# Performance work log

Measured on AMD Instinct MI355X. Metric: run time of the kernel, lower is better.

Reference implementation:

```python
import jax, jax.numpy as jnp
import numpy as np
import math

N = 50000      # nodes
E = 800000     # edges
D = 128        # in/out channels (hidden_dim)
H = 16         # heads
C = D // H     # per-head channels = 8
DH = 4 * D     # mlp hidden = 512
EPS = 1e-5


def layernorm(x, g, b):
    mu = jnp.mean(x, axis=-1, keepdims=True)
    var = jnp.var(x, axis=-1, keepdims=True)
    return (x - mu) * jax.lax.rsqrt(var + EPS) * g + b


def setup_inputs() -> dict:
    key = jax.random.key(0)
    ks = jax.random.split(key, 16)
    s = lambda k, shape, fan: jax.random.normal(k, shape, jnp.float32) / np.sqrt(fan)
    inp = {
        "x": jax.random.normal(ks[0], (N, D), jnp.float32),
        "edge_index": jax.random.randint(ks[1], (2, E), 0, N, jnp.int32),
        "edge_attr": jax.random.normal(ks[2], (E, D), jnp.float32),
        # layer norm 1
        "ln1_g": jnp.ones((D,), jnp.float32), "ln1_b": jnp.zeros((D,), jnp.float32),
        # q/k/v/self projections (in=D, out=H*C=D)
        "wq": s(ks[3], (D, D), D), "bq": jnp.zeros((D,), jnp.float32),
        "wk": s(ks[4], (D, D), D), "bk": jnp.zeros((D,), jnp.float32),
        "wv": s(ks[5], (D, D), D), "bv": jnp.zeros((D,), jnp.float32),
        "ws": s(ks[6], (D, D), D), "bs": jnp.zeros((D,), jnp.float32),
        # edge projection (edge_dim=D -> H*C)
        "we": s(ks[7], (D, D), D), "be": jnp.zeros((D,), jnp.float32),
        # output projection
        "wp": s(ks[8], (D, D), D), "bp": jnp.zeros((D,), jnp.float32),
        # node_dst_mlp: LN -> Linear(D,4D) -> SiLU -> Linear(4D,D)
        "mlp_ln_g": jnp.ones((D,), jnp.float32), "mlp_ln_b": jnp.zeros((D,), jnp.float32),
        "w1": s(ks[9], (D, DH), D), "b1": jnp.zeros((DH,), jnp.float32),
        "w2": s(ks[10], (DH, D), DH), "b2": jnp.zeros((D,), jnp.float32),
    }
    return inp


def reference(x, edge_index, edge_attr, ln1_g, ln1_b, wq, bq, wk, bk, wv, bv,
              ws, bs, we, be, wp, bp, mlp_ln_g, mlp_ln_b, w1, b1, w2, b2):
    src, dst = edge_index[0], edge_index[1]  # message j -> i

    h = layernorm(x, ln1_g, ln1_b)
    q = (h @ wq + bq).reshape(N, H, C)
    k = (h @ wk + bk).reshape(N, H, C)
    v = (h @ wv + bv).reshape(N, H, C)
    x_r = h @ ws + bs                         # [N, D]

    # per-edge gather + edge-feature add
    k_j = k[src] + (edge_attr @ we + be).reshape(E, H, C)  # [E,H,C]
    alpha = jnp.sum(q[dst] * k_j, axis=-1) / math.sqrt(C)  # [E,H]

    # segment softmax over destination nodes
    m = jax.ops.segment_max(alpha, dst, num_segments=N)    # [N,H]
    ex = jnp.exp(alpha - m[dst])
    denom = jax.ops.segment_sum(ex, dst, num_segments=N)   # [N,H]
    alpha = ex / denom[dst]

    # weighted scatter-add aggregation
    msg = v[src] * alpha[..., None]                        # [E,H,C]
    agg = jax.ops.segment_sum(msg, dst, num_segments=N).reshape(N, D)

    out = (agg + x_r) @ wp + bp
    out = out + x                                          # residual to raw input
    mlp_out = jax.nn.silu(layernorm(out, mlp_ln_g, mlp_ln_b) @ w1 + b1) @ w2 + b2
    return mlp_out + out
```

## Files before the change

kernel.cpp:

```cpp
#include <hip/hip_runtime.h>

#define N_NODES 50000
#define N_EDGES 800000
#define D 128
#define H 16
#define DH 512

typedef __attribute__((ext_vector_type(8))) short short8;
typedef __attribute__((ext_vector_type(4))) float f32x4;

static __device__ __forceinline__ unsigned short f2bf(float f) {
    unsigned u = __float_as_uint(f);
    u += 0x7FFF + ((u >> 16) & 1);
    return (unsigned short)(u >> 16);
}
static __device__ __forceinline__ float bf2f(unsigned short u) {
    return __uint_as_float(((unsigned)u) << 16);
}

__global__ void ln_kernel(const float* __restrict__ x, const float* __restrict__ g,
                          const float* __restrict__ b, unsigned short* __restrict__ out, int n) {
    int w = (blockIdx.x * blockDim.x + threadIdx.x) >> 6;
    int lane = threadIdx.x & 63;
    if (w >= n) return;
    float2 v = *(const float2*)(x + (size_t)w * D + lane * 2);
    float s = v.x + v.y, ss = v.x * v.x + v.y * v.y;
#pragma unroll
    for (int off = 32; off; off >>= 1) { s += __shfl_xor(s, off); ss += __shfl_xor(ss, off); }
    float mean = s * (1.0f / D);
    float var = ss * (1.0f / D) - mean * mean;
    float rstd = rsqrtf(var + 1e-5f);
    float2 gv = *(const float2*)(g + lane * 2);
    float2 bv = *(const float2*)(b + lane * 2);
    ushort2 o;
    o.x = f2bf((v.x - mean) * rstd * gv.x + bv.x);
    o.y = f2bf((v.y - mean) * rstd * gv.y + bv.y);
    *(ushort2*)(out + (size_t)w * D + lane * 2) = o;
}

__global__ void prep_kernel(const float* __restrict__ wq, const float* __restrict__ wk,
                            const float* __restrict__ wv, const float* __restrict__ ws,
                            const float* __restrict__ we, const float* __restrict__ wp,
                            const float* __restrict__ w1, const float* __restrict__ w2,
                            const float* __restrict__ bq, const float* __restrict__ bk,
                            const float* __restrict__ bv, const float* __restrict__ bs,
                            unsigned short* __restrict__ wqkvsT, unsigned short* __restrict__ weT,
                            unsigned short* __restrict__ wpT, unsigned short* __restrict__ w1T,
                            unsigned short* __restrict__ w2T, float* __restrict__ bias_qkvs) {
    int idx = blockIdx.x * blockDim.x + threadIdx.x;
    if (idx < 65536) {
        int seg = idx >> 14, r = idx & 16383;
        const float* src = seg == 0 ? wq : seg == 1 ? wk : seg == 2 ? wv : ws;
        int o = r >> 7, i = r & 127;
        wqkvsT[idx] = f2bf(src[i * 128 + o]);
    } else if (idx < 81920) {
        int r = idx - 65536; int o = r >> 7, i = r & 127;
        weT[r] = f2bf(we[i * 128 + o]);
    } else if (idx < 98304) {
        int r = idx - 81920; int o = r >> 7, i = r & 127;
        wpT[r] = f2bf(wp[i * 128 + o]);
    } else if (idx < 163840) {
        int r = idx - 98304; int o = r >> 7, i = r & 127;
        w1T[r] = f2bf(w1[i * 512 + o]);
    } else if (idx < 229376) {
        int r = idx - 163840; int o = r >> 9, i = r & 511;
        w2T[r] = f2bf(w2[i * 128 + o]);
    } else if (idx < 229888) {
        int r = idx - 229376;
        const float* p = r < 128 ? bq : r < 256 ? bk : r < 384 ? bv : bs;
        bias_qkvs[r] = p[r & 127];
    }
}

__global__ void hist_kernel(const int* __restrict__ edge_index, int* __restrict__ counts) {
    int e = blockIdx.x * blockDim.x + threadIdx.x;
    if (e < N_EDGES) atomicAdd(&counts[edge_index[N_EDGES + e]], 1);
}

__global__ void scan1_kernel(const int* __restrict__ counts, int* __restrict__ excl,
                             int* __restrict__ bsum) {
    __shared__ int sm[1024];
    int b = blockIdx.x, tid = threadIdx.x;
    int idx = b * 1024 + tid;
    int v = (idx < N_NODES) ? counts[idx] : 0;
    sm[tid] = v;
    __syncthreads();
    for (int off = 1; off < 1024; off <<= 1) {
        int t = (tid >= off) ? sm[tid - off] : 0;
        __syncthreads();
        sm[tid] += t;
        __syncthreads();
    }
    if (idx < N_NODES) excl[idx] = sm[tid] - v;
    if (tid == 1023) bsum[b] = sm[1023];
}

__global__ void scan2_kernel(int* __restrict__ bsum, int nb) {
    if (threadIdx.x == 0 && blockIdx.x == 0) {
        int run = 0;
        for (int i = 0; i < nb; ++i) { int v = bsum[i]; bsum[i] = run; run += v; }
    }
}

__global__ void scan3_kernel(const int* __restrict__ excl, const int* __restrict__ bsum,
                             int* __restrict__ row_ptr, int* __restrict__ cursor) {
    int b = blockIdx.x, tid = threadIdx.x;
    int idx = b * 1024 + tid;
    if (idx < N_NODES) {
        int v = bsum[b] + excl[idx];
        row_ptr[idx] = v;
        cursor[idx] = v;
    }
    if (idx == 0) row_ptr[N_NODES] = N_EDGES;
}

__global__ void scatter_kernel(const int* __restrict__ edge_index, int* __restrict__ cursor,
                               int* __restrict__ slot_of, int* __restrict__ src_ord) {
    int e = blockIdx.x * blockDim.x + threadIdx.x;
    if (e < N_EDGES) {
        int dst = edge_index[N_EDGES + e];
        int pos = atomicAdd(&cursor[dst], 1);
        slot_of[e] = pos;
        src_ord[pos] = edge_index[e];
    }
}

enum { EPI_F32 = 0, EPI_RESID = 1, EPI_SILU_BF = 2, EPI_ADDOUT = 3, EPI_BF16 = 4 };

template <int KD, int EPI>
__global__ void gemm_kernel(const unsigned short* __restrict__ A, const unsigned short* __restrict__ BT,
                            const float* __restrict__ bias, void* __restrict__ outp,
                            const float* __restrict__ extra, int M, int Nout) {
    int wave = threadIdx.x >> 6, lane = threadIdx.x & 63;
    int lr = lane & 15, lq = lane >> 4;
    int row0 = (blockIdx.x * 4 + wave) * 16;
    int col0 = blockIdx.y * 64;
    int arow = row0 + lr;
    if (arow >= M) arow = M - 1;
    f32x4 z = {0.f, 0.f, 0.f, 0.f};
    f32x4 acc[4] = {z, z, z, z};
#pragma unroll
    for (int t = 0; t < KD / 32; ++t) {
        short8 a = *(const short8*)(A + (size_t)arow * KD + t * 32 + lq * 8);
#pragma unroll
        for (int cf = 0; cf < 4; ++cf) {
            short8 b = *(const short8*)(BT + (size_t)(col0 + cf * 16 + lr) * KD + t * 32 + lq * 8);
            acc[cf] = __builtin_amdgcn_mfma_f32_16x16x32_bf16(a, b, acc[cf], 0, 0, 0);
        }
    }
#pragma unroll
    for (int cf = 0; cf < 4; ++cf) {
        int col = col0 + cf * 16 + lr;
        float bv = bias[col];
#pragma unroll
        for (int r = 0; r < 4; ++r) {
            int row = row0 + lq * 4 + r;
            if (row >= M) continue;
            float v = acc[cf][r] + bv;
            if (EPI == EPI_F32) {
                ((float*)outp)[(size_t)row * Nout + col] = v;
            } else if (EPI == EPI_RESID) {
                ((float*)outp)[(size_t)row * Nout + col] = v + extra[(size_t)row * D + col];
            } else if (EPI == EPI_SILU_BF) {
                float sg = 1.0f / (1.0f + __expf(-v));
                ((unsigned short*)outp)[(size_t)row * Nout + col] = f2bf(v * sg);
            } else if (EPI == EPI_ADDOUT) {
                ((float*)outp)[(size_t)row * Nout + col] = v + extra[(size_t)row * D + col];
            } else {
                ((unsigned short*)outp)[(size_t)row * Nout + col] = f2bf(v);
            }
        }
    }
}

__global__ __launch_bounds__(128)
void edge_score_kernel(const float* __restrict__ edge_attr,
                       const unsigned short* __restrict__ weT,
                       const float* __restrict__ be, const int* __restrict__ edge_index,
                       const int* __restrict__ slot_of,
                       const unsigned short* __restrict__ qkvs,
                       float* __restrict__ qE) {
    __shared__ unsigned short q_lds[32][132];
    __shared__ float s_lds[32][20];
    int wave = threadIdx.x >> 6, lane = threadIdx.x & 63;
    int lr = lane & 15, lq = lane >> 4;
    int w16 = wave * 16;
    int e0w = blockIdx.x * 32 + w16;

    int dstv = edge_index[N_EDGES + e0w + lr];
    int slotv = slot_of[e0w + lr];

    int plane = lane >> 5, h2 = lane & 31;
#pragma unroll
    for (int it = 0; it < 8; ++it) {
        int row16 = it * 2 + plane;
        int dst = __shfl(dstv, row16);
        *(ushort4*)(&q_lds[w16 + row16][h2 * 4]) =
            *(const ushort4*)(qkvs + (size_t)dst * 512 + h2 * 4);
    }

    short8 a[4];
#pragma unroll
    for (int t = 0; t < 4; ++t) {
        const f32x4* p = (const f32x4*)(edge_attr + (size_t)(e0w + lr) * D + t * 32 + lq * 8);
        f32x4 lo = __builtin_nontemporal_load(p);
        f32x4 hi = __builtin_nontemporal_load(p + 1);
        short8 av;
        av[0] = f2bf(lo[0]); av[1] = f2bf(lo[1]); av[2] = f2bf(lo[2]); av[3] = f2bf(lo[3]);
        av[4] = f2bf(hi[0]); av[5] = f2bf(hi[1]); av[6] = f2bf(hi[2]); av[7] = f2bf(hi[3]);
        a[t] = av;
    }
    f32x4 z = {0.f, 0.f, 0.f, 0.f};
    f32x4 acc[8] = {z, z, z, z, z, z, z, z};
#pragma unroll
    for (int cf = 0; cf < 8; ++cf) {
#pragma unroll
        for (int t = 0; t < 4; ++t) {
            short8 b = *(const short8*)(weT + (size_t)(cf * 16 + lr) * D + t * 32 + lq * 8);
            acc[cf] = __builtin_amdgcn_mfma_f32_16x16x32_bf16(a[t], b, acc[cf], 0, 0, 0);
        }
    }

#pragma unroll
    for (int cf = 0; cf < 8; ++cf) {
        int col = cf * 16 + lr;
        float bev = be[col];
#pragma unroll
        for (int r = 0; r < 4; ++r) {
            int el = w16 + lq * 4 + r;
            float qv = bf2f(q_lds[el][col]);
            float p = qv * (acc[cf][r] + bev);
            p += __shfl_xor(p, 1);
            p += __shfl_xor(p, 2);
            p += __shfl_xor(p, 4);
            if ((lr & 7) == 0)
                s_lds[el][cf * 2 + (lr >> 3)] = p;
        }
    }

    int el16 = lane >> 2;
    int slot = __shfl(slotv, el16);
    f32x4 sv = *(const f32x4*)(&s_lds[w16 + el16][(lane & 3) * 4]);
    *(f32x4*)(qE + (size_t)slot * 16 + (lane & 3) * 4) = sv;
}

__global__ void agg_kernel(const int* __restrict__ row_ptr, const int* __restrict__ src_ord,
                           const float* __restrict__ qE, const unsigned short* __restrict__ qkvs,
                           unsigned short* __restrict__ aggxr) {
    int w = (blockIdx.x * blockDim.x + threadIdx.x) >> 6;
    int lane = threadIdx.x & 63;
    if (w >= N_NODES) return;
    int c = lane * 2, h = lane >> 2;
    int s = row_ptr[w], e = row_ptr[w + 1], deg = e - s;
    int src_p = (lane < deg) ? src_ord[s + lane] : 0;
    ushort2 q2 = *(const ushort2*)(qkvs + (size_t)w * 512 + c);
    float qa = bf2f(q2.x), qb = bf2f(q2.y);
    const float scale = 0.35355339059327373f;
    float acc0 = 0.f, acc1 = 0.f, den = 0.f;
    for (int i = 0; i < deg; ++i) {
        int src = (i < 64) ? __shfl(src_p, i) : src_ord[s + i];
        ushort2 k2 = *(const ushort2*)(qkvs + (size_t)src * 512 + 128 + c);
        ushort2 v2 = *(const ushort2*)(qkvs + (size_t)src * 512 + 256 + c);
        float pa = qa * bf2f(k2.x) + qb * bf2f(k2.y);
        pa += __shfl_xor(pa, 1);
        pa += __shfl_xor(pa, 2);
        float qEv = qE[(size_t)(s + i) * 16 + h];
        float ex = __expf((pa + qEv) * scale);
        acc0 += ex * bf2f(v2.x);
        acc1 += ex * bf2f(v2.y);
        den += ex;
    }
    float inv = den > 0.f ? 1.0f / den : 0.f;
    ushort2 x2 = *(const ushort2*)(qkvs + (size_t)w * 512 + 384 + c);
    ushort2 o;
    o.x = f2bf(acc0 * inv + bf2f(x2.x));
    o.y = f2bf(acc1 * inv + bf2f(x2.y));
    *(ushort2*)(aggxr + (size_t)w * D + c) = o;
}

extern "C" void kernel_launch(void* const* d_in, const int* in_sizes, int n_in,
                              void* d_out, int out_size, void* d_ws, size_t ws_size,
                              hipStream_t stream) {
    const float* x = (const float*)d_in[0];
    const int* edge_index = (const int*)d_in[1];
    const float* edge_attr = (const float*)d_in[2];
    const float* ln1_g = (const float*)d_in[3];
    const float* ln1_b = (const float*)d_in[4];
    const float* wq = (const float*)d_in[5];  const float* bq = (const float*)d_in[6];
    const float* wk = (const float*)d_in[7];  const float* bk = (const float*)d_in[8];
    const float* wv = (const float*)d_in[9];  const float* bv = (const float*)d_in[10];
    const float* wsw = (const float*)d_in[11]; const float* bs = (const float*)d_in[12];
    const float* we = (const float*)d_in[13]; const float* be = (const float*)d_in[14];
    const float* wp = (const float*)d_in[15]; const float* bp = (const float*)d_in[16];
    const float* mlp_g = (const float*)d_in[17]; const float* mlp_b = (const float*)d_in[18];
    const float* w1 = (const float*)d_in[19]; const float* b1 = (const float*)d_in[20];
    const float* w2 = (const float*)d_in[21]; const float* b2 = (const float*)d_in[22];

    char* base = (char*)d_ws;
    size_t off = 0;
    auto alloc = [&](size_t bytes) -> char* {
        char* p = base + off;
        off = (off + bytes + 255) & ~(size_t)255;
        return p;
    };
    unsigned short* qkvs   = (unsigned short*)alloc((size_t)N_NODES * 512 * 2);
    float* qE_buf          = (float*)alloc((size_t)N_EDGES * H * 4);
    unsigned short* h_bf   = (unsigned short*)alloc((size_t)N_NODES * D * 2);
    unsigned short* aggxr  = (unsigned short*)alloc((size_t)N_NODES * D * 2);
    float* outbuf          = (float*)alloc((size_t)N_NODES * D * 4);
    unsigned short* ln2_bf = (unsigned short*)alloc((size_t)N_NODES * D * 2);
    unsigned short* silu_bf= (unsigned short*)alloc((size_t)N_NODES * DH * 2);
    int* counts            = (int*)alloc((size_t)N_NODES * 4);
    int* row_ptr           = (int*)alloc((size_t)(N_NODES + 1) * 4);
    int* cursor            = (int*)alloc((size_t)N_NODES * 4);
    int* slot_of           = (int*)alloc((size_t)N_EDGES * 4);
    int* src_ord           = (int*)alloc((size_t)N_EDGES * 4);
    int* excl              = (int*)alloc((size_t)N_NODES * 4);
    int* bsum              = (int*)alloc(64 * 4);
    unsigned short* wqkvsT = (unsigned short*)alloc(512 * 128 * 2);
    unsigned short* weT    = (unsigned short*)alloc(128 * 128 * 2);
    unsigned short* wpT    = (unsigned short*)alloc(128 * 128 * 2);
    unsigned short* w1T    = (unsigned short*)alloc(512 * 128 * 2);
    unsigned short* w2T    = (unsigned short*)alloc(128 * 512 * 2);
    float* bias_qkvs       = (float*)alloc(512 * 4);

    const int NB = (N_NODES + 1023) / 1024;

    prep_kernel<<<898, 256, 0, stream>>>(wq, wk, wv, wsw, we, wp, w1, w2, bq, bk, bv, bs,
                                         wqkvsT, weT, wpT, w1T, w2T, bias_qkvs);

    (void)hipMemsetAsync(counts, 0, (size_t)N_NODES * 4, stream);
    hist_kernel<<<(N_EDGES + 255) / 256, 256, 0, stream>>>(edge_index, counts);
    scan1_kernel<<<NB, 1024, 0, stream>>>(counts, excl, bsum);
    scan2_kernel<<<1, 64, 0, stream>>>(bsum, NB);
    scan3_kernel<<<NB, 1024, 0, stream>>>(excl, bsum, row_ptr, cursor);
    scatter_kernel<<<(N_EDGES + 255) / 256, 256, 0, stream>>>(edge_index, cursor, slot_of, src_ord);

    ln_kernel<<<(N_NODES + 3) / 4, 256, 0, stream>>>(x, ln1_g, ln1_b, h_bf, N_NODES);

    dim3 g_node((N_NODES + 63) / 64, 8);
    gemm_kernel<128, EPI_BF16><<<g_node, 256, 0, stream>>>(h_bf, wqkvsT, bias_qkvs, qkvs, nullptr, N_NODES, 512);

    edge_score_kernel<<<N_EDGES / 32, 128, 0, stream>>>(edge_attr, weT, be, edge_index, slot_of, qkvs, qE_buf);

    agg_kernel<<<(N_NODES + 3) / 4, 256, 0, stream>>>(row_ptr, src_ord, qE_buf, qkvs, aggxr);

    dim3 g_out((N_NODES + 63) / 64, 2);
    gemm_kernel<128, EPI_RESID><<<g_out, 256, 0, stream>>>(aggxr, wpT, bp, outbuf, x, N_NODES, 128);

    ln_kernel<<<(N_NODES + 3) / 4, 256, 0, stream>>>(outbuf, mlp_g, mlp_b, ln2_bf, N_NODES);

    dim3 g_mlp1((N_NODES + 63) / 64, 8);
    gemm_kernel<128, EPI_SILU_BF><<<g_mlp1, 256, 0, stream>>>(ln2_bf, w1T, b1, silu_bf, nullptr, N_NODES, 512);

    dim3 g_mlp2((N_NODES + 63) / 64, 2);
    gemm_kernel<512, EPI_ADDOUT><<<g_mlp2, 256, 0, stream>>>(silu_bf, w2T, b2, (float*)d_out, outbuf, N_NODES, 128);
}
```

Before: 676.3 us.

## Split edge projection GEMM from score computation into two kernels

The fused edge-score kernel is split in two. One kernel runs the edge_attr @ we GEMM, processing 32 rows per wave, and writes a bf16 intermediate E_bf. A second kernel gathers q[dst], adds the bias, computes per-head dot products and scatters the scores to their CSR slots. The intent is to simplify each kernel and improve MFMA/occupancy, at the cost of writing and re-reading a 200MB bf16 intermediate. Rounding E to bf16 before the bias add and dot product also slightly changes numerics.

After: 737.7 us. 1.09x slower.

```diff
diff --git a/kernel.cpp b/kernel.cpp
--- a/kernel.cpp
+++ b/kernel.cpp
@@ -173,75 +173,78 @@
     }
 }
 
-__global__ __launch_bounds__(128)
-void edge_score_kernel(const float* __restrict__ edge_attr,
-                       const unsigned short* __restrict__ weT,
-                       const float* __restrict__ be, const int* __restrict__ edge_index,
-                       const int* __restrict__ slot_of,
-                       const unsigned short* __restrict__ qkvs,
-                       float* __restrict__ qE) {
-    __shared__ unsigned short q_lds[32][132];
-    __shared__ float s_lds[32][20];
+__global__ __launch_bounds__(256)
+void e_gemm_kernel(const float* __restrict__ edge_attr,
+                   const unsigned short* __restrict__ weT,
+                   unsigned short* __restrict__ E_bf) {
     int wave = threadIdx.x >> 6, lane = threadIdx.x & 63;
     int lr = lane & 15, lq = lane >> 4;
-    int w16 = wave * 16;
-    int e0w = blockIdx.x * 32 + w16;
-
-    int dstv = edge_index[N_EDGES + e0w + lr];
-    int slotv = slot_of[e0w + lr];
-
-    int plane = lane >> 5, h2 = lane & 31;
-#pragma unroll
-    for (int it = 0; it < 8; ++it) {
-        int row16 = it * 2 + plane;
-        int dst = __shfl(dstv, row16);
-        *(ushort4*)(&q_lds[w16 + row16][h2 * 4]) =
-            *(const ushort4*)(qkvs + (size_t)dst * 512 + h2 * 4);
-    }
-
-    short8 a[4];
+    int row0 = (blockIdx.x * 4 + wave) * 32;
+
+    short8 a0[4], a1[4];
 #pragma unroll
     for (int t = 0; t < 4; ++t) {
-        const f32x4* p = (const f32x4*)(edge_attr + (size_t)(e0w + lr) * D + t * 32 + lq * 8);
-        f32x4 lo = __builtin_nontemporal_load(p);
-        f32x4 hi = __builtin_nontemporal_load(p + 1);
-        short8 av;
-        av[0] = f2bf(lo[0]); av[1] = f2bf(lo[1]); av[2] = f2bf(lo[2]); av[3] = f2bf(lo[3]);
-        av[4] = f2bf(hi[0]); av[5] = f2bf(hi[1]); av[6] = f2bf(hi[2]); av[7] = f2bf(hi[3]);
-        a[t] = av;
+        const f32x4* p0 = (const f32x4*)(edge_attr + (size_t)(row0 + lr) * D + t * 32 + lq * 8);
+        const f32x4* p1 = (const f32x4*)(edge_attr + (size_t)(row0 + 16 + lr) * D + t * 32 + lq * 8);
+        f32x4 lo0 = __builtin_nontemporal_load(p0);
+        f32x4 hi0 = __builtin_nontemporal_load(p0 + 1);
+        f32x4 lo1 = __builtin_nontemporal_load(p1);
+        f32x4 hi1 = __builtin_nontemporal_load(p1 + 1);
+        short8 v0, v1;
+        v0[0] = f2bf(lo0[0]); v0[1] = f2bf(lo0[1]); v0[2] = f2bf(lo0[2]); v0[3] = f2bf(lo0[3]);
+        v0[4] = f2bf(hi0[0]); v0[5] = f2bf(hi0[1]); v0[6] = f2bf(hi0[2]); v0[7] = f2bf(hi0[3]);
+        v1[0] = f2bf(lo1[0]); v1[1] = f2bf(lo1[1]); v1[2] = f2bf(lo1[2]); v1[3] = f2bf(lo1[3]);
+        v1[4] = f2bf(hi1[0]); v1[5] = f2bf(hi1[1]); v1[6] = f2bf(hi1[2]); v1[7] = f2bf(hi1[3]);
+        a0[t] = v0; a1[t] = v1;
     }
     f32x4 z = {0.f, 0.f, 0.f, 0.f};
-    f32x4 acc[8] = {z, z, z, z, z, z, z, z};
+    f32x4 acc0[8] = {z, z, z, z, z, z, z, z};
+    f32x4 acc1[8] = {z, z, z, z, z, z, z, z};
 #pragma unroll
     for (int cf = 0; cf < 8; ++cf) {
 #pragma unroll
         for (int t = 0; t < 4; ++t) {
             short8 b = *(const short8*)(weT + (size_t)(cf * 16 + lr) * D + t * 32 + lq * 8);
-            acc[cf] = __builtin_amdgcn_mfma_f32_16x16x32_bf16(a[t], b, acc[cf], 0, 0, 0);
+            acc0[cf] = __builtin_amdgcn_mfma_f32_16x16x32_bf16(a0[t], b, acc0[cf], 0, 0, 0);
+            acc1[cf] = __builtin_amdgcn_mfma_f32_16x16x32_bf16(a1[t], b, acc1[cf], 0, 0, 0);
         }
     }
-
 #pragma unroll
     for (int cf = 0; cf < 8; ++cf) {
         int col = cf * 16 + lr;
-        float bev = be[col];
 #pragma unroll
         for (int r = 0; r < 4; ++r) {
-            int el = w16 + lq * 4 + r;
-            float qv = bf2f(q_lds[el][col]);
-            float p = qv * (acc[cf][r] + bev);
-            p += __shfl_xor(p, 1);
-            p += __shfl_xor(p, 2);
-            p += __shfl_xor(p, 4);
-            if ((lr & 7) == 0)
-                s_lds[el][cf * 2 + (lr >> 3)] = p;
+            int row = row0 + lq * 4 + r;
+            E_bf[(size_t)row * D + col] = f2bf(acc0[cf][r]);
+            E_bf[(size_t)(row + 16) * D + col] = f2bf(acc1[cf][r]);
         }
     }
-
-    int el16 = lane >> 2;
-    int slot = __shfl(slotv, el16);
-    f32x4 sv = *(const f32x4*)(&s_lds[w16 + el16][(lane & 3) * 4]);
-    *(f32x4*)(qE + (size_t)slot * 16 + (lane & 3) * 4) = sv;
+}
+
+__global__ __launch_bounds__(256)
+void score_kernel(const unsigned short* __restrict__ E_bf, const float* __restrict__ be,
+                  const int* __restrict__ edge_index, const int* __restrict__ slot_of,
+                  const unsigned short* __restrict__ qkvs, float* __restrict__ qE) {
+    int gw = (blockIdx.x * blockDim.x + threadIdx.x) >> 6;
+    int lane = threadIdx.x & 63;
+    int c2 = lane * 2, h = lane >> 2;
+    int base_e = gw * 16;
+    int dstv = edge_index[N_EDGES + base_e + (lane & 15)];
+    int slotv = slot_of[base_e + (lane & 15)];
+    float2 bev = *(const float2*)(be + c2);
+#pragma unroll
+    for (int i = 0; i < 16; ++i) {
+        int e = base_e + i;
+        int dst = __shfl(dstv, i);
+        int slot = __shfl(slotv, i);
+        ushort2 q2 = *(const ushort2*)(qkvs + (size_t)dst * 512 + c2);
+        ushort2 E2 = *(const ushort2*)(E_bf + (size_t)e * D + c2);
+        float p = bf2f(q2.x) * (bf2f(E2.x) + bev.x) + bf2f(q2.y) * (bf2f(E2.y) + bev.y);
+        p += __shfl_xor(p, 1);
+        p += __shfl_xor(p, 2);
+        if ((lane & 3) == 0)
+            qE[(size_t)slot * 16 + h] = p;
+    }
 }
 
 __global__ void agg_kernel(const int* __restrict__ row_ptr, const int* __restrict__ src_ord,
@@ -305,6 +308,7 @@
     };
     unsigned short* qkvs   = (unsigned short*)alloc((size_t)N_NODES * 512 * 2);
     float* qE_buf          = (float*)alloc((size_t)N_EDGES * H * 4);
+    unsigned short* E_bf   = (unsigned short*)alloc((size_t)N_EDGES * D * 2);
     unsigned short* h_bf   = (unsigned short*)alloc((size_t)N_NODES * D * 2);
     unsigned short* aggxr  = (unsigned short*)alloc((size_t)N_NODES * D * 2);
     float* outbuf          = (float*)alloc((size_t)N_NODES * D * 4);
@@ -341,7 +345,8 @@
     dim3 g_node((N_NODES + 63) / 64, 8);
     gemm_kernel<128, EPI_BF16><<<g_node, 256, 0, stream>>>(h_bf, wqkvsT, bias_qkvs, qkvs, nullptr, N_NODES, 512);
 
-    edge_score_kernel<<<N_EDGES / 32, 128, 0, stream>>>(edge_attr, weT, be, edge_index, slot_of, qkvs, qE_buf);
+    e_gemm_kernel<<<N_EDGES / 128, 256, 0, stream>>>(edge_attr, weT, E_bf);
+    score_kernel<<<N_EDGES / 64, 256, 0, stream>>>(E_bf, be, edge_index, slot_of, qkvs, qE_buf);
 
     agg_kernel<<<(N_NODES + 3) / 4, 256, 0, stream>>>(row_ptr, src_ord, qE_buf, qkvs, aggxr);
 
```

## Fuse layernorms into GEMMs, interleave K/V layout, prefetch edge loads

Applied to the files above, without the earlier changes.

Removes both standalone layernorm kernels and computes LN inside the GEMM A-tile load, so the normalized bf16 intermediates are never written to or read back from memory. Each of the 8 column blocks recomputes the LN of the same fp32 rows, which adds redundant reads and math. The QKVS output is stored with K and V interleaved per channel, so the aggregation loop fetches both with one ushort4 load instead of two. In the edge score kernel, the edge_attr loads and q gathers are issued into registers before the LDS stores, to overlap their memory latency.

Result: slower. 711.7 us (+5.2%).

```diff
diff --git a/kernel.cpp b/kernel.cpp
--- a/kernel.cpp
+++ b/kernel.cpp
@@ -16,26 +16,6 @@
 }
 static __device__ __forceinline__ float bf2f(unsigned short u) {
     return __uint_as_float(((unsigned)u) << 16);
-}
-
-__global__ void ln_kernel(const float* __restrict__ x, const float* __restrict__ g,
-                          const float* __restrict__ b, unsigned short* __restrict__ out, int n) {
-    int w = (blockIdx.x * blockDim.x + threadIdx.x) >> 6;
-    int lane = threadIdx.x & 63;
-    if (w >= n) return;
-    float2 v = *(const float2*)(x + (size_t)w * D + lane * 2);
-    float s = v.x + v.y, ss = v.x * v.x + v.y * v.y;
-#pragma unroll
-    for (int off = 32; off; off >>= 1) { s += __shfl_xor(s, off); ss += __shfl_xor(ss, off); }
-    float mean = s * (1.0f / D);
-    float var = ss * (1.0f / D) - mean * mean;
-    float rstd = rsqrtf(var + 1e-5f);
-    float2 gv = *(const float2*)(g + lane * 2);
-    float2 bv = *(const float2*)(b + lane * 2);
-    ushort2 o;
-    o.x = f2bf((v.x - mean) * rstd * gv.x + bv.x);
-    o.y = f2bf((v.y - mean) * rstd * gv.y + bv.y);
-    *(ushort2*)(out + (size_t)w * D + lane * 2) = o;
 }
 
 __global__ void prep_kernel(const float* __restrict__ wq, const float* __restrict__ wk,
@@ -125,7 +105,7 @@
     }
 }
 
-enum { EPI_F32 = 0, EPI_RESID = 1, EPI_SILU_BF = 2, EPI_ADDOUT = 3, EPI_BF16 = 4 };
+enum { EPI_F32 = 0, EPI_RESID = 1, EPI_SILU_BF = 2, EPI_ADDOUT = 3, EPI_BF16 = 4, EPI_QKVS = 5 };
 
 template <int KD, int EPI>
 __global__ void gemm_kernel(const unsigned short* __restrict__ A, const unsigned short* __restrict__ BT,
@@ -173,6 +153,83 @@
     }
 }
 
+template <int EPI>
+__global__ void gemm_ln_kernel(const float* __restrict__ A, const unsigned short* __restrict__ BT,
+                               const float* __restrict__ bias, const float* __restrict__ lng,
+                               const float* __restrict__ lnb, void* __restrict__ outp,
+                               int M, int Nout) {
+    int wave = threadIdx.x >> 6, lane = threadIdx.x & 63;
+    int lr = lane & 15, lq = lane >> 4;
+    int row0 = (blockIdx.x * 4 + wave) * 16;
+    int col0 = blockIdx.y * 64;
+    int arow = row0 + lr;
+    if (arow >= M) arow = M - 1;
+
+    f32x4 xa[8];
+    float s = 0.f, ss = 0.f;
+#pragma unroll
+    for (int t = 0; t < 4; ++t) {
+        const f32x4* p = (const f32x4*)(A + (size_t)arow * D + t * 32 + lq * 8);
+        xa[2 * t] = p[0];
+        xa[2 * t + 1] = p[1];
+#pragma unroll
+        for (int j = 0; j < 4; ++j) {
+            s += xa[2 * t][j] + xa[2 * t + 1][j];
+            ss += xa[2 * t][j] * xa[2 * t][j] + xa[2 * t + 1][j] * xa[2 * t + 1][j];
+        }
+    }
+    s += __shfl_xor(s, 16); s += __shfl_xor(s, 32);
+    ss += __shfl_xor(ss, 16); ss += __shfl_xor(ss, 32);
+    float mean = s * (1.0f / D);
+    float rstd = rsqrtf(ss * (1.0f / D) - mean * mean + 1e-5f);
+
+    short8 a[4];
+#pragma unroll
+    for (int t = 0; t < 4; ++t) {
+        const f32x4* gp = (const f32x4*)(lng + t * 32 + lq * 8);
+        const f32x4* bp = (const f32x4*)(lnb + t * 32 + lq * 8);
+        f32x4 g0 = gp[0], g1 = gp[1], b0 = bp[0], b1 = bp[1];
+        short8 av;
+#pragma unroll
+        for (int j = 0; j < 4; ++j) {
+            av[j] = f2bf((xa[2 * t][j] - mean) * rstd * g0[j] + b0[j]);
+            av[j + 4] = f2bf((xa[2 * t + 1][j] - mean) * rstd * g1[j] + b1[j]);
+        }
+        a[t] = av;
+    }
+
+    f32x4 z = {0.f, 0.f, 0.f, 0.f};
+    f32x4 acc[4] = {z, z, z, z};
+#pragma unroll
+    for (int t = 0; t < 4; ++t) {
+#pragma unroll
+        for (int cf = 0; cf < 4; ++cf) {
+            short8 b = *(const short8*)(BT + (size_t)(col0 + cf * 16 + lr) * D + t * 32 + lq * 8);
+            acc[cf] = __builtin_amdgcn_mfma_f32_16x16x32_bf16(a[t], b, acc[cf], 0, 0, 0);
+        }
+    }
+#pragma unroll
+    for (int cf = 0; cf < 4; ++cf) {
+        int col = col0 + cf * 16 + lr;
+        float bv = bias[col];
+#pragma unroll
+        for (int r = 0; r < 4; ++r) {
+            int row = row0 + lq * 4 + r;
+            if (row >= M) continue;
+            float v = acc[cf][r] + bv;
+            if (EPI == EPI_QKVS) {
+                int seg = col >> 7, c = col & 127;
+                size_t o = (seg == 0) ? (size_t)c : (seg == 1) ? (size_t)(128 + 2 * c)
+                         : (seg == 2) ? (size_t)(129 + 2 * c) : (size_t)(384 + c);
+                ((unsigned short*)outp)[(size_t)row * 512 + o] = f2bf(v);
+            } else {
+                float sg = 1.0f / (1.0f + __expf(-v));
+                ((unsigned short*)outp)[(size_t)row * Nout + col] = f2bf(v * sg);
+            }
+        }
+    }
+}
+
 __global__ __launch_bounds__(128)
 void edge_score_kernel(const float* __restrict__ edge_attr,
                        const unsigned short* __restrict__ weT,
@@ -186,30 +243,38 @@
     int lr = lane & 15, lq = lane >> 4;
     int w16 = wave * 16;
     int e0w = blockIdx.x * 32 + w16;
+    int plane = lane >> 5, h2 = lane & 31;
+
+    f32x4 lo[4], hi[4];
+#pragma unroll
+    for (int t = 0; t < 4; ++t) {
+        const f32x4* p = (const f32x4*)(edge_attr + (size_t)(e0w + lr) * D + t * 32 + lq * 8);
+        lo[t] = __builtin_nontemporal_load(p);
+        hi[t] = __builtin_nontemporal_load(p + 1);
+    }
 
     int dstv = edge_index[N_EDGES + e0w + lr];
     int slotv = slot_of[e0w + lr];
-
-    int plane = lane >> 5, h2 = lane & 31;
+    ushort4 qreg[8];
 #pragma unroll
     for (int it = 0; it < 8; ++it) {
-        int row16 = it * 2 + plane;
-        int dst = __shfl(dstv, row16);
-        *(ushort4*)(&q_lds[w16 + row16][h2 * 4]) =
-            *(const ushort4*)(qkvs + (size_t)dst * 512 + h2 * 4);
+        int dst = __shfl(dstv, it * 2 + plane);
+        qreg[it] = *(const ushort4*)(qkvs + (size_t)dst * 512 + h2 * 4);
     }
 
     short8 a[4];
 #pragma unroll
     for (int t = 0; t < 4; ++t) {
-        const f32x4* p = (const f32x4*)(edge_attr + (size_t)(e0w + lr) * D + t * 32 + lq * 8);
-        f32x4 lo = __builtin_nontemporal_load(p);
-        f32x4 hi = __builtin_nontemporal_load(p + 1);
         short8 av;
-        av[0] = f2bf(lo[0]); av[1] = f2bf(lo[1]); av[2] = f2bf(lo[2]); av[3] = f2bf(lo[3]);
-        av[4] = f2bf(hi[0]); av[5] = f2bf(hi[1]); av[6] = f2bf(hi[2]); av[7] = f2bf(hi[3]);
+        av[0] = f2bf(lo[t][0]); av[1] = f2bf(lo[t][1]); av[2] = f2bf(lo[t][2]); av[3] = f2bf(lo[t][3]);
+        av[4] = f2bf(hi[t][0]); av[5] = f2bf(hi[t][1]); av[6] = f2bf(hi[t][2]); av[7] = f2bf(hi[t][3]);
         a[t] = av;
     }
+
+#pragma unroll
+    for (int it = 0; it < 8; ++it)
+        *(ushort4*)(&q_lds[w16 + it * 2 + plane][h2 * 4]) = qreg[it];
+
     f32x4 z = {0.f, 0.f, 0.f, 0.f};
     f32x4 acc[8] = {z, z, z, z, z, z, z, z};
 #pragma unroll
@@ -259,15 +324,14 @@
     float acc0 = 0.f, acc1 = 0.f, den = 0.f;
     for (int i = 0; i < deg; ++i) {
         int src = (i < 64) ? __shfl(src_p, i) : src_ord[s + i];
-        ushort2 k2 = *(const ushort2*)(qkvs + (size_t)src * 512 + 128 + c);
-        ushort2 v2 = *(const ushort2*)(qkvs + (size_t)src * 512 + 256 + c);
-        float pa = qa * bf2f(k2.x) + qb * bf2f(k2.y);
+        ushort4 kv = *(const ushort4*)(qkvs + (size_t)src * 512 + 128 + (size_t)c * 2);
+        float pa = qa * bf2f(kv.x) + qb * bf2f(kv.z);
         pa += __shfl_xor(pa, 1);
         pa += __shfl_xor(pa, 2);
         float qEv = qE[(size_t)(s + i) * 16 + h];
         float ex = __expf((pa + qEv) * scale);
-        acc0 += ex * bf2f(v2.x);
-        acc1 += ex * bf2f(v2.y);
+        acc0 += ex * bf2f(kv.y);
+        acc1 += ex * bf2f(kv.w);
         den += ex;
     }
     float inv = den > 0.f ? 1.0f / den : 0.f;
@@ -305,10 +369,8 @@
     };
     unsigned short* qkvs   = (unsigned short*)alloc((size_t)N_NODES * 512 * 2);
     float* qE_buf          = (float*)alloc((size_t)N_EDGES * H * 4);
-    unsigned short* h_bf   = (unsigned short*)alloc((size_t)N_NODES * D * 2);
     unsigned short* aggxr  = (unsigned short*)alloc((size_t)N_NODES * D * 2);
     float* outbuf          = (float*)alloc((size_t)N_NODES * D * 4);
-    unsigned short* ln2_bf = (unsigned short*)alloc((size_t)N_NODES * D * 2);
     unsigned short* silu_bf= (unsigned short*)alloc((size_t)N_NODES * DH * 2);
     int* counts            = (int*)alloc((size_t)N_NODES * 4);
     int* row_ptr           = (int*)alloc((size_t)(N_NODES + 1) * 4);
@@ -336,10 +398,9 @@
     scan3_kernel<<<NB, 1024, 0, stream>>>(excl, bsum, row_ptr, cursor);
     scatter_kernel<<<(N_EDGES + 255) / 256, 256, 0, stream>>>(edge_index, cursor, slot_of, src_ord);
 
-    ln_kernel<<<(N_NODES + 3) / 4, 256, 0, stream>>>(x, ln1_g, ln1_b, h_bf, N_NODES);
-
     dim3 g_node((N_NODES + 63) / 64, 8);
-    gemm_kernel<128, EPI_BF16><<<g_node, 256, 0, stream>>>(h_bf, wqkvsT, bias_qkvs, qkvs, nullptr, N_NODES, 512);
+    gemm_ln_kernel<EPI_QKVS><<<g_node, 256, 0, stream>>>(x, wqkvsT, bias_qkvs, ln1_g, ln1_b,
+                                                         qkvs, N_NODES, 512);
 
     edge_score_kernel<<<N_EDGES / 32, 128, 0, stream>>>(edge_attr, weT, be, edge_index, slot_of, qkvs, qE_buf);
 
@@ -348,10 +409,9 @@
     dim3 g_out((N_NODES + 63) / 64, 2);
     gemm_kernel<128, EPI_RESID><<<g_out, 256, 0, stream>>>(aggxr, wpT, bp, outbuf, x, N_NODES, 128);
 
-    ln_kernel<<<(N_NODES + 3) / 4, 256, 0, stream>>>(outbuf, mlp_g, mlp_b, ln2_bf, N_NODES);
-
     dim3 g_mlp1((N_NODES + 63) / 64, 8);
-    gemm_kernel<128, EPI_SILU_BF><<<g_mlp1, 256, 0, stream>>>(ln2_bf, w1T, b1, silu_bf, nullptr, N_NODES, 512);
+    gemm_ln_kernel<EPI_SILU_BF><<<g_mlp1, 256, 0, stream>>>(outbuf, w1T, b1, mlp_g, mlp_b,
+                                                            silu_bf, N_NODES, 512);
 
     dim3 g_mlp2((N_NODES + 63) / 64, 2);
     gemm_kernel<512, EPI_ADDOUT><<<g_mlp2, 256, 0, stream>>>(silu_bf, w2T, b2, (float*)d_out, outbuf, N_NODES, 128);
```

## Interleave K/V in qkvs, hoist edge loads, split edge-score launch by cache hint

Applied to the files above, without the earlier changes.

The QKVS GEMM epilogue now writes K and V interleaved per channel, so the aggregation loop fetches both with a single 8-byte gather per source instead of two 4-byte gathers. The edge-score kernel issues its edge_attr loads before the q gathers and stages q through registers before writing LDS, to overlap more memory latency. The edge-score work is also split into two launches: the first half uses nontemporal loads and the second half uses normal loads, probably to keep part of edge_attr cached across calls. This adds an extra launch, uses more registers, and makes the GEMM stores more scattered.

Measured after the change: 710.3 us. 1.05x slower.

```diff
diff --git a/kernel.cpp b/kernel.cpp
--- a/kernel.cpp
+++ b/kernel.cpp
@@ -125,7 +125,7 @@
     }
 }
 
-enum { EPI_F32 = 0, EPI_RESID = 1, EPI_SILU_BF = 2, EPI_ADDOUT = 3, EPI_BF16 = 4 };
+enum { EPI_F32 = 0, EPI_RESID = 1, EPI_SILU_BF = 2, EPI_ADDOUT = 3, EPI_BF16 = 4, EPI_QKVS = 5 };
 
 template <int KD, int EPI>
 __global__ void gemm_kernel(const unsigned short* __restrict__ A, const unsigned short* __restrict__ BT,
@@ -166,6 +166,11 @@
                 ((unsigned short*)outp)[(size_t)row * Nout + col] = f2bf(v * sg);
             } else if (EPI == EPI_ADDOUT) {
                 ((float*)outp)[(size_t)row * Nout + col] = v + extra[(size_t)row * D + col];
+            } else if (EPI == EPI_QKVS) {
+                int seg = col >> 7, c = col & 127;
+                size_t o = (seg == 0) ? (size_t)c : (seg == 1) ? (size_t)(128 + 2 * c)
+                         : (seg == 2) ? (size_t)(129 + 2 * c) : (size_t)(384 + c);
+                ((unsigned short*)outp)[(size_t)row * 512 + o] = f2bf(v);
             } else {
                 ((unsigned short*)outp)[(size_t)row * Nout + col] = f2bf(v);
             }
@@ -173,43 +178,57 @@
     }
 }
 
+template <bool NT>
 __global__ __launch_bounds__(128)
 void edge_score_kernel(const float* __restrict__ edge_attr,
                        const unsigned short* __restrict__ weT,
                        const float* __restrict__ be, const int* __restrict__ edge_index,
                        const int* __restrict__ slot_of,
                        const unsigned short* __restrict__ qkvs,
-                       float* __restrict__ qE) {
+                       float* __restrict__ qE, int e_base) {
     __shared__ unsigned short q_lds[32][132];
     __shared__ float s_lds[32][20];
     int wave = threadIdx.x >> 6, lane = threadIdx.x & 63;
     int lr = lane & 15, lq = lane >> 4;
     int w16 = wave * 16;
-    int e0w = blockIdx.x * 32 + w16;
+    int e0w = e_base + blockIdx.x * 32 + w16;
+    int plane = lane >> 5, h2 = lane & 31;
+
+    f32x4 lo[4], hi[4];
+#pragma unroll
+    for (int t = 0; t < 4; ++t) {
+        const f32x4* p = (const f32x4*)(edge_attr + (size_t)(e0w + lr) * D + t * 32 + lq * 8);
+        if (NT) {
+            lo[t] = __builtin_nontemporal_load(p);
+            hi[t] = __builtin_nontemporal_load(p + 1);
+        } else {
+            lo[t] = p[0];
+            hi[t] = p[1];
+        }
+    }
 
     int dstv = edge_index[N_EDGES + e0w + lr];
     int slotv = slot_of[e0w + lr];
-
-    int plane = lane >> 5, h2 = lane & 31;
+    ushort4 qreg[8];
 #pragma unroll
     for (int it = 0; it < 8; ++it) {
-        int row16 = it * 2 + plane;
-        int dst = __shfl(dstv, row16);
-        *(ushort4*)(&q_lds[w16 + row16][h2 * 4]) =
-            *(const ushort4*)(qkvs + (size_t)dst * 512 + h2 * 4);
+        int dst = __shfl(dstv, it * 2 + plane);
+        qreg[it] = *(const ushort4*)(qkvs + (size_t)dst * 512 + h2 * 4);
     }
 
     short8 a[4];
 #pragma unroll
     for (int t = 0; t < 4; ++t) {
-        const f32x4* p = (const f32x4*)(edge_attr + (size_t)(e0w + lr) * D + t * 32 + lq * 8);
-        f32x4 lo = __builtin_nontemporal_load(p);
-        f32x4 hi = __builtin_nontemporal_load(p + 1);
         short8 av;
-        av[0] = f2bf(lo[0]); av[1] = f2bf(lo[1]); av[2] = f2bf(lo[2]); av[3] = f2bf(lo[3]);
-        av[4] = f2bf(hi[0]); av[5] = f2bf(hi[1]); av[6] = f2bf(hi[2]); av[7] = f2bf(hi[3]);
+        av[0] = f2bf(lo[t][0]); av[1] = f2bf(lo[t][1]); av[2] = f2bf(lo[t][2]); av[3] = f2bf(lo[t][3]);
+        av[4] = f2bf(hi[t][0]); av[5] = f2bf(hi[t][1]); av[6] = f2bf(hi[t][2]); av[7] = f2bf(hi[t][3]);
         a[t] = av;
     }
+
+#pragma unroll
+    for (int it = 0; it < 8; ++it)
+        *(ushort4*)(&q_lds[w16 + it * 2 + plane][h2 * 4]) = qreg[it];
+
     f32x4 z = {0.f, 0.f, 0.f, 0.f};
     f32x4 acc[8] = {z, z, z, z, z, z, z, z};
 #pragma unroll
@@ -259,15 +278,14 @@
     float acc0 = 0.f, acc1 = 0.f, den = 0.f;
     for (int i = 0; i < deg; ++i) {
         int src = (i < 64) ? __shfl(src_p, i) : src_ord[s + i];
-        ushort2 k2 = *(const ushort2*)(qkvs + (size_t)src * 512 + 128 + c);
-        ushort2 v2 = *(const ushort2*)(qkvs + (size_t)src * 512 + 256 + c);
-        float pa = qa * bf2f(k2.x) + qb * bf2f(k2.y);
+        ushort4 kv = *(const ushort4*)(qkvs + (size_t)src * 512 + 128 + (size_t)c * 2);
+        float pa = qa * bf2f(kv.x) + qb * bf2f(kv.z);
         pa += __shfl_xor(pa, 1);
         pa += __shfl_xor(pa, 2);
         float qEv = qE[(size_t)(s + i) * 16 + h];
         float ex = __expf((pa + qEv) * scale);
-        acc0 += ex * bf2f(v2.x);
-        acc1 += ex * bf2f(v2.y);
+        acc0 += ex * bf2f(kv.y);
+        acc1 += ex * bf2f(kv.w);
         den += ex;
     }
     float inv = den > 0.f ? 1.0f / den : 0.f;
@@ -339,9 +357,12 @@
     ln_kernel<<<(N_NODES + 3) / 4, 256, 0, stream>>>(x, ln1_g, ln1_b, h_bf, N_NODES);
 
     dim3 g_node((N_NODES + 63) / 64, 8);
-    gemm_kernel<128, EPI_BF16><<<g_node, 256, 0, stream>>>(h_bf, wqkvsT, bias_qkvs, qkvs, nullptr, N_NODES, 512);
-
-    edge_score_kernel<<<N_EDGES / 32, 128, 0, stream>>>(edge_attr, weT, be, edge_index, slot_of, qkvs, qE_buf);
+    gemm_kernel<128, EPI_QKVS><<<g_node, 256, 0, stream>>>(h_bf, wqkvsT, bias_qkvs, qkvs, nullptr, N_NODES, 512);
+
+    edge_score_kernel<true><<<N_EDGES / 2 / 32, 128, 0, stream>>>(
+        edge_attr, weT, be, edge_index, slot_of, qkvs, qE_buf, 0);
+    edge_score_kernel<false><<<N_EDGES / 2 / 32, 128, 0, stream>>>(
+        edge_attr, weT, be, edge_index, slot_of, qkvs, qE_buf, N_EDGES / 2);
 
     agg_kernel<<<(N_NODES + 3) / 4, 256, 0, stream>>>(row_ptr, src_ord, qE_buf, qkvs, aggxr);
 
```
